# Performance work log

Hardware: AMD Instinct MI355X
Metric: run time of the kernel (lower is better)

Reference implementation:

```python
import jax, jax.numpy as jnp
import numpy as np

N = 100000   # num nodes
E = 1200000  # num edges
D = 64       # embedding dim
K = 3        # propagation hops (alpha has K+1 entries)


def setup_inputs() -> dict:
    key = jax.random.key(0)
    k1, k2, k3 = jax.random.split(key, 3)
    edge_index = jax.random.randint(k1, (2, E), 0, N, dtype=jnp.int64)
    weight = jax.random.normal(k2, (N, D), dtype=jnp.float32)
    alpha = jax.random.uniform(k3, (K + 1,), dtype=jnp.float32)
    return {"edge_index": edge_index, "weight": weight, "alpha": alpha}


def reference(edge_index, weight, alpha):
    row = edge_index[0]  # source j
    col = edge_index[1]  # target i
    # symmetric normalization: in-degree over col, deg^-1/2 with inf -> 0
    deg = jax.ops.segment_sum(jnp.ones((E,), dtype=weight.dtype), col, num_segments=N)
    dinv = jnp.where(deg == 0, 0.0, deg ** -0.5)
    edge_w = dinv[row] * dinv[col]  # [E]

    out = weight * alpha[0]
    x = weight
    for k in range(1, K + 1):
        # gather-scale-scatter propagation hop
        msg = edge_w[:, None] * x[row]                      # [E, D]
        x = jax.ops.segment_sum(msg, col, num_segments=N)   # [N, D]
        out = out + x * alpha[k]

    # per-edge link scores: dot(out[src], out[dst])
    return jnp.sum(out[row] * out[col], axis=-1)  # [E]
```

## Files before the change

kernel.cpp:

```cpp
#include <hip/hip_runtime.h>
#include <hip/hip_bf16.h>

#define GN 100000
#define GE 1200000
#define GD 64
#define NG 256
#define CPG 391
#define CAP 6144


__global__ void detect_kernel(const void* __restrict__ w,
                              const void* __restrict__ edge,
                              int* __restrict__ flags) {
    __shared__ int s_badw, s_edgenz;
    if (threadIdx.x == 0) { s_badw = 0; s_edgenz = 0; }
    __syncthreads();
    const unsigned short* wh = (const unsigned short*)w;
    const unsigned int*   ei = (const unsigned int*)edge;
    int badw = 0, edgenz = 0;
    for (int i = threadIdx.x; i < 4096; i += 256) {
        unsigned int bits = ((unsigned int)wh[i]) << 16;
        float v = __uint_as_float(bits);
        if (!(fabsf(v) <= 100.0f)) badw = 1;
        if ((i & 1) == 1 && ei[i] != 0u) edgenz = 1;
    }
    if (badw)   atomicOr(&s_badw, 1);
    if (edgenz) atomicOr(&s_edgenz, 1);
    __syncthreads();
    if (threadIdx.x == 0) {
        flags[0] = s_badw ? 0 : 1;
        flags[1] = s_edgenz ? 0 : 1;
    }
}

__device__ __forceinline__ int ld_row(const int* __restrict__ edge, int e, int e64) {
    return e64 ? edge[2 * (size_t)e] : edge[e];
}
__device__ __forceinline__ int ld_col(const int* __restrict__ edge, int e, int e64) {
    return e64 ? edge[2 * ((size_t)GE + (size_t)e)] : edge[(size_t)GE + (size_t)e];
}
__device__ __forceinline__ float ld_f(const void* __restrict__ p, size_t i, int bf16f) {
    if (bf16f) return __bfloat162float(((const __hip_bfloat16*)p)[i]);
    return ((const float*)p)[i];
}

__device__ __forceinline__ float bf_lo(unsigned u) { return __uint_as_float(u << 16); }
__device__ __forceinline__ float bf_hi(unsigned u) { return __uint_as_float(u & 0xFFFF0000u); }
__device__ __forceinline__ unsigned bf16bits(float f) {
    __hip_bfloat16 h = __float2bfloat16(f);
    unsigned short s;
    __builtin_memcpy(&s, &h, 2);
    return (unsigned)s;
}

__global__ void p1_kernel(const int* __restrict__ edge, const int* __restrict__ flags,
                          int* __restrict__ gcount, unsigned* __restrict__ bucket,
                          int E, int chunk) {
    __shared__ int cnt[NG];
    __shared__ int base[NG];
    int t = threadIdx.x;
    int e64 = flags[1];
    cnt[t] = 0;
    __syncthreads();
    int lo = blockIdx.x * chunk;
    int hiE = min(lo + chunk, E);
    for (int e = lo + t; e < hiE; e += 256) {
        int c = ld_col(edge, e, e64);
        int r = ld_row(edge, e, e64);
        if ((unsigned)c < (unsigned)GN && (unsigned)r < (unsigned)GN)
            atomicAdd(&cnt[c / CPG], 1);
    }
    __syncthreads();
    int cv = cnt[t];
    base[t] = (cv > 0) ? atomicAdd(&gcount[t], cv) : 0;
    __syncthreads();
    cnt[t] = 0;
    __syncthreads();
    for (int e = lo + t; e < hiE; e += 256) {
        int c = ld_col(edge, e, e64);
        int r = ld_row(edge, e, e64);
        if ((unsigned)c < (unsigned)GN && (unsigned)r < (unsigned)GN) {
            int g = c / CPG;
            int idx = base[g] + atomicAdd(&cnt[g], 1);
            if (idx < CAP)
                bucket[(size_t)g * CAP + idx] = ((unsigned)(c - g * CPG) << 17) | (unsigned)r;
        }
    }
}

__global__ void gscan_kernel(const int* __restrict__ gcount, int* __restrict__ groupBase) {
    __shared__ int s[NG];
    int t = threadIdx.x;
    int v = gcount[t]; if (v > CAP) v = CAP;
    s[t] = v;
    __syncthreads();
    for (int off = 1; off < NG; off <<= 1) {
        int u = (t >= off) ? s[t - off] : 0;
        __syncthreads();
        s[t] += u;
        __syncthreads();
    }
    groupBase[t] = s[t] - v;
}

__global__ void p2_kernel(const unsigned* __restrict__ bucket, const int* __restrict__ gcount,
                          const int* __restrict__ groupBase,
                          int* __restrict__ rowptr, float* __restrict__ dinv,
                          int* __restrict__ csr) {
    int g = blockIdx.x;
    int t = threadIdx.x;
    int m = gcount[g]; if (m > CAP) m = CAP;
    int gb = groupBase[g];
    __shared__ int hist[512];
    __shared__ int s[512];
    hist[t] = 0; hist[t + 256] = 0;
    __syncthreads();
    const unsigned* bk = bucket + (size_t)g * CAP;
    for (int idx = t; idx < m; idx += 256)
        atomicAdd(&hist[bk[idx] >> 17], 1);
    __syncthreads();
    int h0 = hist[t], h1 = hist[t + 256];
    s[t] = h0; s[t + 256] = h1;
    __syncthreads();
    for (int off = 1; off < 512; off <<= 1) {
        int v0 = (t >= off) ? s[t - off] : 0;
        int v1 = (t + 256 >= off) ? s[t + 256 - off] : 0;
        __syncthreads();
        s[t] += v0; s[t + 256] += v1;
        __syncthreads();
    }
    int col0 = g * CPG + t;
    int col1 = col0 + 256;
    if (col0 < GN) {
        rowptr[col0] = gb + s[t];
        dinv[col0] = (h0 > 0) ? rsqrtf((float)h0) : 0.0f;
    }
    if (t + 256 < CPG && col1 < GN) {
        rowptr[col1] = gb + s[t + 256];
        dinv[col1] = (h1 > 0) ? rsqrtf((float)h1) : 0.0f;
    }
    __syncthreads();
    hist[t] = s[t] - h0;
    hist[t + 256] = s[t + 256] - h1;
    __syncthreads();
    for (int idx = t; idx < m; idx += 256) {
        unsigned u = bk[idx];
        int cl = u >> 17;
        int r  = (int)(u & 0x1FFFFu);
        int pos = gb + atomicAdd(&hist[cl], 1);
        csr[pos] = r;
    }
}

__global__ void init_kernel(const void* __restrict__ w, const void* __restrict__ alpha,
                            const int* __restrict__ flags,
                            __hip_bfloat16* __restrict__ X, __hip_bfloat16* __restrict__ OUT,
                            int n) {
    int i = 4 * (blockIdx.x * blockDim.x + threadIdx.x);
    int wbf = flags[0];
    if (i < n) {
        float a0 = ld_f(alpha, 0, wbf);
        #pragma unroll
        for (int q = 0; q < 4; ++q) {
            float v = ld_f(w, i + q, wbf);
            X[i + q] = __float2bfloat16(v);
            OUT[i + q] = __float2bfloat16(a0 * v);
        }
    }
}

__global__ void gather_kernel(const __hip_bfloat16* __restrict__ X,
                              __hip_bfloat16* __restrict__ Y,
                              __hip_bfloat16* __restrict__ OUT,
                              const int* __restrict__ rowptr, const int* __restrict__ csr,
                              const float* __restrict__ dinv,
                              const void* __restrict__ alpha, const int* __restrict__ flags,
                              int k, int store_y, int N) {
    int t = blockIdx.x * blockDim.x + threadIdx.x;
    int node = __builtin_amdgcn_readfirstlane(t >> 6);
    if (node >= N) return;
    int lane = t & 63;
    int h = lane >> 5;
    int i = lane & 31;
    int beg = node ? rowptr[node - 1] : 0;
    int end = rowptr[node];
    float dc = dinv[node];
    float ax0 = 0.0f, ay0 = 0.0f, ax1 = 0.0f, ay1 = 0.0f;
    float ax2 = 0.0f, ay2 = 0.0f, ax3 = 0.0f, ay3 = 0.0f;
    int j = beg;
    for (; j + 8 <= end; j += 8) {
        int r0 = csr[j + 0 + h];
        int r1 = csr[j + 2 + h];
        int r2 = csr[j + 4 + h];
        int r3 = csr[j + 6 + h];
        float w0 = dinv[r0]; float w1 = dinv[r1];
        float w2 = dinv[r2]; float w3 = dinv[r3];
        unsigned u0 = *(const unsigned*)(X + (size_t)r0 * GD + 2 * i);
        unsigned u1 = *(const unsigned*)(X + (size_t)r1 * GD + 2 * i);
        unsigned u2 = *(const unsigned*)(X + (size_t)r2 * GD + 2 * i);
        unsigned u3 = *(const unsigned*)(X + (size_t)r3 * GD + 2 * i);
        ax0 = fmaf(w0, bf_lo(u0), ax0); ay0 = fmaf(w0, bf_hi(u0), ay0);
        ax1 = fmaf(w1, bf_lo(u1), ax1); ay1 = fmaf(w1, bf_hi(u1), ay1);
        ax2 = fmaf(w2, bf_lo(u2), ax2); ay2 = fmaf(w2, bf_hi(u2), ay2);
        ax3 = fmaf(w3, bf_lo(u3), ax3); ay3 = fmaf(w3, bf_hi(u3), ay3);
    }
    for (; j + 2 <= end; j += 2) {
        int r = csr[j + h];
        float w = dinv[r];
        unsigned u = *(const unsigned*)(X + (size_t)r * GD + 2 * i);
        ax0 = fmaf(w, bf_lo(u), ax0); ay0 = fmaf(w, bf_hi(u), ay0);
    }
    if (j < end) {
        int r = csr[j];
        float w = (h == 0) ? dinv[r] : 0.0f;
        unsigned u = *(const unsigned*)(X + (size_t)r * GD + 2 * i);
        ax0 = fmaf(w, bf_lo(u), ax0); ay0 = fmaf(w, bf_hi(u), ay0);
    }
    float accx = (ax0 + ax1) + (ax2 + ax3);
    float accy = (ay0 + ay1) + (ay2 + ay3);
    accx += __shfl_xor(accx, 32, 64);
    accy += __shfl_xor(accy, 32, 64);
    accx *= dc; accy *= dc;
    float a = ld_f(alpha, k, flags[0]);
    if (h == 0) {
        __hip_bfloat16* yp = Y + (size_t)node * GD + 2 * i;
        __hip_bfloat16* op = OUT + (size_t)node * GD + 2 * i;
        if (store_y) {
            unsigned pack = (bf16bits(accy) << 16) | bf16bits(accx);
            *(unsigned*)yp = pack;
        }
        unsigned uo = *(const unsigned*)op;
        float ox = fmaf(a, accx, bf_lo(uo));
        float oy = fmaf(a, accy, bf_hi(uo));
        *(unsigned*)op = (bf16bits(oy) << 16) | bf16bits(ox);
    }
}

__device__ __forceinline__ float dot2_bf16(unsigned ua, unsigned ub) {
    return fmaf(bf_lo(ua), bf_lo(ub), bf_hi(ua) * bf_hi(ub));
}

__global__ void dot_kernel(const __hip_bfloat16* __restrict__ OUT,
                           const int* __restrict__ edge, const int* __restrict__ flags,
                           void* __restrict__ res, int E) {
    int t = blockIdx.x * blockDim.x + threadIdx.x;
    int e = t >> 2;
    int sub = t & 3;
    if (e >= E) return;
    int e64 = flags[1];
    int wbf = flags[0];
    int r = ld_row(edge, e, e64);
    int c = ld_col(edge, e, e64);
    float p = 0.0f;
    if ((unsigned)r < (unsigned)GN && (unsigned)c < (unsigned)GN) {
        const uint4* pa = (const uint4*)(OUT + (size_t)r * GD + sub * 16);
        const uint4* pb = (const uint4*)(OUT + (size_t)c * GD + sub * 16);
        uint4 a0 = pa[0], a1 = pa[1];
        uint4 b0 = pb[0], b1 = pb[1];
        p = ((dot2_bf16(a0.x, b0.x) + dot2_bf16(a0.y, b0.y)) +
             (dot2_bf16(a0.z, b0.z) + dot2_bf16(a0.w, b0.w))) +
            ((dot2_bf16(a1.x, b1.x) + dot2_bf16(a1.y, b1.y)) +
             (dot2_bf16(a1.z, b1.z) + dot2_bf16(a1.w, b1.w)));
    }
    p += __shfl_down(p, 2, 4);
    p += __shfl_down(p, 1, 4);
    if (sub == 0) {
        if (wbf) ((__hip_bfloat16*)res)[e] = __float2bfloat16(p);
        else     ((float*)res)[e] = p;
    }
}

extern "C" void kernel_launch(void* const* d_in, const int* in_sizes, int n_in,
                              void* d_out, int out_size, void* d_ws, size_t ws_size,
                              hipStream_t stream) {
    const int E = GE, N = GN, ND = GN * GD;

    const void* edge   = d_in[0];
    const void* weight = d_in[1];
    const void* alpha  = d_in[2];

    char* ws = (char*)d_ws;
    int*      flags     = (int*)ws;      ws += 256;
    int*      gcount    = (int*)ws;      ws += 1024;
    int*      groupBase = (int*)ws;      ws += 1024;
    float*    dinv      = (float*)ws;    ws += (((size_t)N * 4 + 255) / 256) * 256;
    int*      rowptr    = (int*)ws;      ws += (((size_t)N * 4 + 255) / 256) * 256;
    unsigned* bucket    = (unsigned*)ws; ws += (size_t)NG * CAP * 4;
    int*      csr       = (int*)ws;      ws += (size_t)E * 4;
    __hip_bfloat16* X   = (__hip_bfloat16*)ws; ws += (size_t)ND * 2;
    __hip_bfloat16* Y   = (__hip_bfloat16*)ws; ws += (size_t)ND * 2;
    __hip_bfloat16* OUT = (__hip_bfloat16*)ws; ws += (size_t)ND * 2;

    const int B = 256;

    detect_kernel<<<1, 256, 0, stream>>>(weight, edge, flags);

    hipMemsetAsync(gcount, 0, NG * 4, stream);
    {
        const int P1B = 256;
        const int chunk = (E + P1B - 1) / P1B;
        p1_kernel<<<P1B, 256, 0, stream>>>((const int*)edge, flags, gcount, bucket, E, chunk);
    }
    gscan_kernel<<<1, NG, 0, stream>>>(gcount, groupBase);
    p2_kernel<<<NG, 256, 0, stream>>>(bucket, gcount, groupBase, rowptr, dinv, csr);

    init_kernel<<<(ND / 4 + B - 1) / B, B, 0, stream>>>(weight, alpha, flags, X, OUT, ND);

    const int ggrid = (int)(((size_t)N * 64 + B - 1) / B);
    gather_kernel<<<ggrid, B, 0, stream>>>(X, Y, OUT, rowptr, csr, dinv, alpha, flags, 1, 1, N);
    gather_kernel<<<ggrid, B, 0, stream>>>(Y, X, OUT, rowptr, csr, dinv, alpha, flags, 2, 1, N);
    gather_kernel<<<ggrid, B, 0, stream>>>(X, Y, OUT, rowptr, csr, dinv, alpha, flags, 3, 0, N);

    dot_kernel<<<(int)(((size_t)E * 4 + B - 1) / B), B, 0, stream>>>(OUT, (const int*)edge, flags, d_out, E);
}
```

Measured before the change: 305.0 us.

## Widen gather loads to 8 bytes and fold scan and memset into neighbors

The gather kernel now splits each wavefront into four 16-lane groups. Each lane loads 8 bytes (four bf16 values) per neighbor row, with 16 neighbors in flight per iteration and tails handled by clamped, masked loads instead of separate remainder loops. The group prefix scan moves into every p2 block, which drops one launch, and the gcount memset moves into detect_kernel, which drops a memset. This adds redundant scan work in each block and wasted masked lanes on low-degree nodes.

```diff
diff --git a/kernel.cpp b/kernel.cpp
--- a/kernel.cpp
+++ b/kernel.cpp
@@ -11,9 +11,10 @@
 
 __global__ void detect_kernel(const void* __restrict__ w,
                               const void* __restrict__ edge,
-                              int* __restrict__ flags) {
+                              int* __restrict__ flags, int* __restrict__ gcount) {
     __shared__ int s_badw, s_edgenz;
     if (threadIdx.x == 0) { s_badw = 0; s_edgenz = 0; }
+    gcount[threadIdx.x] = 0;
     __syncthreads();
     const unsigned short* wh = (const unsigned short*)w;
     const unsigned int*   ei = (const unsigned int*)edge;
@@ -88,33 +89,27 @@
     }
 }
 
-__global__ void gscan_kernel(const int* __restrict__ gcount, int* __restrict__ groupBase) {
-    __shared__ int s[NG];
-    int t = threadIdx.x;
-    int v = gcount[t]; if (v > CAP) v = CAP;
-    s[t] = v;
-    __syncthreads();
-    for (int off = 1; off < NG; off <<= 1) {
-        int u = (t >= off) ? s[t - off] : 0;
-        __syncthreads();
-        s[t] += u;
-        __syncthreads();
-    }
-    groupBase[t] = s[t] - v;
-}
-
 __global__ void p2_kernel(const unsigned* __restrict__ bucket, const int* __restrict__ gcount,
-                          const int* __restrict__ groupBase,
                           int* __restrict__ rowptr, float* __restrict__ dinv,
                           int* __restrict__ csr) {
     int g = blockIdx.x;
     int t = threadIdx.x;
-    int m = gcount[g]; if (m > CAP) m = CAP;
-    int gb = groupBase[g];
+    __shared__ int gs[NG];
     __shared__ int hist[512];
     __shared__ int s[512];
+    int gv = gcount[t]; if (gv > CAP) gv = CAP;
+    gs[t] = gv;
     hist[t] = 0; hist[t + 256] = 0;
     __syncthreads();
+    for (int off = 1; off < NG; off <<= 1) {
+        int u = (t >= off) ? gs[t - off] : 0;
+        __syncthreads();
+        gs[t] += u;
+        __syncthreads();
+    }
+    int mg = gcount[g]; if (mg > CAP) mg = CAP;
+    int gb = gs[g] - mg;
+    int m = mg;
     const unsigned* bk = bucket + (size_t)g * CAP;
     for (int idx = t; idx < m; idx += 256)
         atomicAdd(&hist[bk[idx] >> 17], 1);
@@ -180,59 +175,60 @@
     int node = __builtin_amdgcn_readfirstlane(t >> 6);
     if (node >= N) return;
     int lane = t & 63;
-    int h = lane >> 5;
-    int i = lane & 31;
+    int h = lane >> 4;
+    int i = lane & 15;
     int beg = node ? rowptr[node - 1] : 0;
     int end = rowptr[node];
     float dc = dinv[node];
-    float ax0 = 0.0f, ay0 = 0.0f, ax1 = 0.0f, ay1 = 0.0f;
-    float ax2 = 0.0f, ay2 = 0.0f, ax3 = 0.0f, ay3 = 0.0f;
-    int j = beg;
-    for (; j + 8 <= end; j += 8) {
-        int r0 = csr[j + 0 + h];
-        int r1 = csr[j + 2 + h];
-        int r2 = csr[j + 4 + h];
-        int r3 = csr[j + 6 + h];
-        float w0 = dinv[r0]; float w1 = dinv[r1];
-        float w2 = dinv[r2]; float w3 = dinv[r3];
-        unsigned u0 = *(const unsigned*)(X + (size_t)r0 * GD + 2 * i);
-        unsigned u1 = *(const unsigned*)(X + (size_t)r1 * GD + 2 * i);
-        unsigned u2 = *(const unsigned*)(X + (size_t)r2 * GD + 2 * i);
-        unsigned u3 = *(const unsigned*)(X + (size_t)r3 * GD + 2 * i);
-        ax0 = fmaf(w0, bf_lo(u0), ax0); ay0 = fmaf(w0, bf_hi(u0), ay0);
-        ax1 = fmaf(w1, bf_lo(u1), ax1); ay1 = fmaf(w1, bf_hi(u1), ay1);
-        ax2 = fmaf(w2, bf_lo(u2), ax2); ay2 = fmaf(w2, bf_hi(u2), ay2);
-        ax3 = fmaf(w3, bf_lo(u3), ax3); ay3 = fmaf(w3, bf_hi(u3), ay3);
-    }
-    for (; j + 2 <= end; j += 2) {
-        int r = csr[j + h];
-        float w = dinv[r];
-        unsigned u = *(const unsigned*)(X + (size_t)r * GD + 2 * i);
-        ax0 = fmaf(w, bf_lo(u), ax0); ay0 = fmaf(w, bf_hi(u), ay0);
-    }
-    if (j < end) {
-        int r = csr[j];
-        float w = (h == 0) ? dinv[r] : 0.0f;
-        unsigned u = *(const unsigned*)(X + (size_t)r * GD + 2 * i);
-        ax0 = fmaf(w, bf_lo(u), ax0); ay0 = fmaf(w, bf_hi(u), ay0);
-    }
-    float accx = (ax0 + ax1) + (ax2 + ax3);
-    float accy = (ay0 + ay1) + (ay2 + ay3);
-    accx += __shfl_xor(accx, 32, 64);
-    accy += __shfl_xor(accy, 32, 64);
-    accx *= dc; accy *= dc;
     float a = ld_f(alpha, k, flags[0]);
+    size_t obase = (size_t)node * GD + 4 * i;
+    uint2 uo = *(const uint2*)(OUT + obase);
+    float f0 = 0.0f, f1 = 0.0f, f2 = 0.0f, f3 = 0.0f;
+    for (int j = beg; j < end; j += 16) {
+        int i0 = j + 0 + h;  int i1 = j + 4 + h;
+        int i2 = j + 8 + h;  int i3 = j + 12 + h;
+        int last = end - 1;
+        int r0 = csr[min(i0, last)];
+        int r1 = csr[min(i1, last)];
+        int r2 = csr[min(i2, last)];
+        int r3 = csr[min(i3, last)];
+        float w0 = (i0 < end) ? dinv[r0] : 0.0f;
+        float w1 = (i1 < end) ? dinv[r1] : 0.0f;
+        float w2 = (i2 < end) ? dinv[r2] : 0.0f;
+        float w3 = (i3 < end) ? dinv[r3] : 0.0f;
+        uint2 u0 = *(const uint2*)(X + (size_t)r0 * GD + 4 * i);
+        uint2 u1 = *(const uint2*)(X + (size_t)r1 * GD + 4 * i);
+        uint2 u2 = *(const uint2*)(X + (size_t)r2 * GD + 4 * i);
+        uint2 u3 = *(const uint2*)(X + (size_t)r3 * GD + 4 * i);
+        f0 = fmaf(w0, bf_lo(u0.x), f0); f1 = fmaf(w0, bf_hi(u0.x), f1);
+        f2 = fmaf(w0, bf_lo(u0.y), f2); f3 = fmaf(w0, bf_hi(u0.y), f3);
+        f0 = fmaf(w1, bf_lo(u1.x), f0); f1 = fmaf(w1, bf_hi(u1.x), f1);
+        f2 = fmaf(w1, bf_lo(u1.y), f2); f3 = fmaf(w1, bf_hi(u1.y), f3);
+        f0 = fmaf(w2, bf_lo(u2.x), f0); f1 = fmaf(w2, bf_hi(u2.x), f1);
+        f2 = fmaf(w2, bf_lo(u2.y), f2); f3 = fmaf(w2, bf_hi(u2.y), f3);
+        f0 = fmaf(w3, bf_lo(u3.x), f0); f1 = fmaf(w3, bf_hi(u3.x), f1);
+        f2 = fmaf(w3, bf_lo(u3.y), f2); f3 = fmaf(w3, bf_hi(u3.y), f3);
+    }
+    f0 += __shfl_xor(f0, 16, 64); f0 += __shfl_xor(f0, 32, 64);
+    f1 += __shfl_xor(f1, 16, 64); f1 += __shfl_xor(f1, 32, 64);
+    f2 += __shfl_xor(f2, 16, 64); f2 += __shfl_xor(f2, 32, 64);
+    f3 += __shfl_xor(f3, 16, 64); f3 += __shfl_xor(f3, 32, 64);
+    f0 *= dc; f1 *= dc; f2 *= dc; f3 *= dc;
     if (h == 0) {
-        __hip_bfloat16* yp = Y + (size_t)node * GD + 2 * i;
-        __hip_bfloat16* op = OUT + (size_t)node * GD + 2 * i;
         if (store_y) {
-            unsigned pack = (bf16bits(accy) << 16) | bf16bits(accx);
-            *(unsigned*)yp = pack;
+            uint2 p;
+            p.x = (bf16bits(f1) << 16) | bf16bits(f0);
+            p.y = (bf16bits(f3) << 16) | bf16bits(f2);
+            *(uint2*)(Y + obase) = p;
         }
-        unsigned uo = *(const unsigned*)op;
-        float ox = fmaf(a, accx, bf_lo(uo));
-        float oy = fmaf(a, accy, bf_hi(uo));
-        *(unsigned*)op = (bf16bits(oy) << 16) | bf16bits(ox);
+        float o0 = fmaf(a, f0, bf_lo(uo.x));
+        float o1 = fmaf(a, f1, bf_hi(uo.x));
+        float o2 = fmaf(a, f2, bf_lo(uo.y));
+        float o3 = fmaf(a, f3, bf_hi(uo.y));
+        uint2 q;
+        q.x = (bf16bits(o1) << 16) | bf16bits(o0);
+        q.y = (bf16bits(o3) << 16) | bf16bits(o2);
+        *(uint2*)(OUT + obase) = q;
     }
 }
 
@@ -282,7 +278,6 @@
     char* ws = (char*)d_ws;
     int*      flags     = (int*)ws;      ws += 256;
     int*      gcount    = (int*)ws;      ws += 1024;
-    int*      groupBase = (int*)ws;      ws += 1024;
     float*    dinv      = (float*)ws;    ws += (((size_t)N * 4 + 255) / 256) * 256;
     int*      rowptr    = (int*)ws;      ws += (((size_t)N * 4 + 255) / 256) * 256;
     unsigned* bucket    = (unsigned*)ws; ws += (size_t)NG * CAP * 4;
@@ -293,16 +288,14 @@
 
     const int B = 256;
 
-    detect_kernel<<<1, 256, 0, stream>>>(weight, edge, flags);
-
-    hipMemsetAsync(gcount, 0, NG * 4, stream);
+    detect_kernel<<<1, 256, 0, stream>>>(weight, edge, flags, gcount);
+
     {
         const int P1B = 256;
         const int chunk = (E + P1B - 1) / P1B;
         p1_kernel<<<P1B, 256, 0, stream>>>((const int*)edge, flags, gcount, bucket, E, chunk);
     }
-    gscan_kernel<<<1, NG, 0, stream>>>(gcount, groupBase);
-    p2_kernel<<<NG, 256, 0, stream>>>(bucket, gcount, groupBase, rowptr, dinv, csr);
+    p2_kernel<<<NG, 256, 0, stream>>>(bucket, gcount, rowptr, dinv, csr);
 
     init_kernel<<<(ND / 4 + B - 1) / B, B, 0, stream>>>(weight, alpha, flags, X, OUT, ND);
 
```

New measurement: 286.9 us. 1.06x faster.
